# Kernel tuning notes

Hardware: AMD Instinct MI355X
Metric: run time of the kernel (lower is better)

The kernel has to match this reference:

```python
import jax, jax.numpy as jnp
import numpy as np

B, S, D, H = 2, 2048, 1024, 16
HD = D // H  # head_dim = 64
LN_EPS = 1e-5


def setup_inputs() -> dict:
    key = jax.random.key(0)
    ks = jax.random.split(key, 14)
    w = 0.02  # weight init scale
    return {
        "q": jax.random.normal(ks[0], (B, S, D), jnp.float32),
        "k": jax.random.normal(ks[1], (B, S, D), jnp.float32),
        "v": jax.random.normal(ks[2], (B, S, D), jnp.float32),
        "mask": jnp.zeros((B, 1, S, S), dtype=bool),
        "training": 0,
        "wq_w": jax.random.normal(ks[3], (D, D), jnp.float32) * w,
        "wq_b": jnp.zeros((D,), jnp.float32),
        "wk_w": jax.random.normal(ks[4], (D, D), jnp.float32) * w,
        "wk_b": jnp.zeros((D,), jnp.float32),
        "wv_w": jax.random.normal(ks[5], (D, D), jnp.float32) * w,
        "wv_b": jnp.zeros((D,), jnp.float32),
        "wo_w": jax.random.normal(ks[6], (D, D), jnp.float32) * w,
        "wo_b": jnp.zeros((D,), jnp.float32),
        "ln_g": jnp.ones((D,), jnp.float32),
        "ln_b": jnp.zeros((D,), jnp.float32),
    }


def _linear(x, w, b):
    # torch nn.Linear: x @ W.T + b, W is [out, in]
    return jnp.einsum('bsd,od->bso', x, w) + b


def _split_heads(x):
    b, s, _ = x.shape
    return x.reshape(b, s, H, HD).transpose(0, 2, 1, 3)  # [B,H,S,HD]


def reference(q, k, v, mask, training, wq_w, wq_b, wk_w, wk_b, wv_w, wv_b,
              wo_w, wo_b, ln_g, ln_b):
    residual = q
    Q = _split_heads(_linear(q, wq_w, wq_b))
    K = _split_heads(_linear(k, wk_w, wk_b))
    V = _split_heads(_linear(v, wv_w, wv_b))
    # source computes sqrt(dk) in float16, then adds 1e-8
    dk = jnp.sqrt(jnp.asarray(HD, jnp.float16)).astype(jnp.float32) + 1e-8
    score = jnp.einsum('bhqd,bhkd->bhqk', Q, K) / dk  # [B,H,S,S]
    # NOTE: source applies NO softmax; masked score is used directly.
    attn = jnp.where(mask, -jnp.inf, score)
    ctx = jnp.einsum('bhqk,bhkd->bhqd', attn, V)  # [B,H,S,HD]
    b, _, s, _ = ctx.shape
    ctx = ctx.transpose(0, 2, 1, 3).reshape(b, s, D)  # [B,S,D]
    o = _linear(ctx, wo_w, wo_b)
    # dropout is identity in eval mode
    x = residual + o
    mu = jnp.mean(x, axis=-1, keepdims=True)
    var = jnp.mean(jnp.square(x - mu), axis=-1, keepdims=True)
    return ln_g * (x - mu) * jax.lax.rsqrt(var + LN_EPS) + ln_b
```

## Files before the change

kernel.cpp:

```cpp
#include <hip/hip_runtime.h>


typedef __bf16 bf16;
typedef __bf16 bf16x8 __attribute__((ext_vector_type(8)));
typedef float f32x4 __attribute__((ext_vector_type(4)));

#define MFMA16(a, b, c) __builtin_amdgcn_mfma_f32_16x16x32_bf16(a, b, c, 0, 0, 0)

__device__ __forceinline__ bf16x8 ld8(const bf16* p) { return *(const bf16x8*)p; }

__device__ __forceinline__ void gload16(const void* g, void* l) {
  __builtin_amdgcn_global_load_lds((__attribute__((address_space(1))) void*)(g),
                                   (__attribute__((address_space(3))) void*)(l), 16, 0, 0);
}

__global__ __launch_bounds__(256) void cvt_kernel(
    const float* __restrict__ q, const float* __restrict__ k, const float* __restrict__ v,
    const float* __restrict__ wq, const float* __restrict__ wk, const float* __restrict__ wv,
    bf16* __restrict__ dst) {
  const int bid = blockIdx.x;
  const float* s; size_t dof; int x;
  if (bid < 6144) {
    const int y = bid >> 11; x = bid & 2047;
    s = (y == 0) ? q : (y == 1 ? k : v);
    dof = (size_t)y * 4194304u;
  } else {
    const int idx = bid - 6144; const int y = idx >> 9; x = idx & 511;
    s = (y == 0) ? wq : (y == 1 ? wk : wv);
    dof = 12582912u + (size_t)y * 1048576u;
  }
  const size_t i = ((size_t)x * 256 + threadIdx.x) * 8;
  f32x4 a = *(const f32x4*)(s + i);
  f32x4 b = *(const f32x4*)(s + i + 4);
  bf16x8 o;
  o[0] = (bf16)a[0]; o[1] = (bf16)a[1]; o[2] = (bf16)a[2]; o[3] = (bf16)a[3];
  o[4] = (bf16)b[0]; o[5] = (bf16)b[1]; o[6] = (bf16)b[2]; o[7] = (bf16)b[3];
  *(bf16x8*)(dst + dof + i) = o;
}

__global__ __launch_bounds__(128, 2) void gemm_proj_f(
    const bf16* __restrict__ Aall, const bf16* __restrict__ Wall,
    const float* __restrict__ bq, const float* __restrict__ bk, const float* __restrict__ bv,
    bf16* __restrict__ Call) {
  __shared__ __align__(128) char lds[32768];
  const int z = blockIdx.y;
  const int wg = blockIdx.x;
  const int swz = ((wg & 7) << 5) + (wg >> 3);
  const int n0 = (swz & 7) * 128, m0 = (swz >> 3) * 128;
  const bf16* A = Aall + (size_t)z * 4194304u;
  const bf16* W = Wall + (size_t)z * 1048576u;
  const float* bias = (z == 0) ? bq : (z == 1 ? bk : bv);
  bf16* C = Call + (size_t)z * 4194304u;

  const int t = threadIdx.x;
  const int l = t & 63, wid = t >> 6;
  const int r16 = l & 15, kg = l >> 4;
  const int wbase = wid << 10;

  const bf16* ap[4]; const bf16* bp[4]; int adst[4], bdst[4];
#pragma unroll
  for (int p = 0; p < 4; p++) {
    const int row = p * 32 + (t >> 2);
    const int c = (t & 3) ^ (row & 3) ^ ((row >> 2) & 3);
    ap[p] = A + (size_t)(m0 + row) * 1024 + c * 8;
    bp[p] = W + (size_t)(n0 + row) * 1024 + c * 8;
    adst[p] = p * 2048 + wbase;
    bdst[p] = 8192 + p * 2048 + wbase;
  }
  int aoff[8], boff[4];
#pragma unroll
  for (int i = 0; i < 8; i++) {
    const int row = i * 16 + r16;
    aoff[i] = row * 64 + ((kg ^ (row & 3) ^ ((row >> 2) & 3)) << 4);
  }
#pragma unroll
  for (int j = 0; j < 4; j++) {
    const int row = wid * 64 + j * 16 + r16;
    boff[j] = 8192 + row * 64 + ((kg ^ (row & 3) ^ ((row >> 2) & 3)) << 4);
  }

  f32x4 acc[8][4] = {};
#pragma unroll
  for (int p = 0; p < 4; p++) { gload16(ap[p], lds + adst[p]); gload16(bp[p], lds + bdst[p]); }
  __syncthreads();

  int buf = 0;
  for (int kt = 0; kt < 32; kt++) {
    if (kt < 31) {
      char* d = lds + ((buf ^ 1) << 14);
#pragma unroll
      for (int p = 0; p < 4; p++) {
        gload16(ap[p] + (kt + 1) * 32, d + adst[p]);
        gload16(bp[p] + (kt + 1) * 32, d + bdst[p]);
      }
    }
    const char* lb = lds + (buf << 14);
    bf16x8 bv_[4];
#pragma unroll
    for (int j = 0; j < 4; j++) bv_[j] = *(const bf16x8*)(lb + boff[j]);
#pragma unroll
    for (int i = 0; i < 8; i++) {
      bf16x8 av = *(const bf16x8*)(lb + aoff[i]);
#pragma unroll
      for (int j = 0; j < 4; j++) acc[i][j] = MFMA16(av, bv_[j], acc[i][j]);
    }
    __syncthreads();
    buf ^= 1;
  }

#pragma unroll
  for (int j = 0; j < 4; j++) {
    const int col = n0 + wid * 64 + j * 16 + r16;
    const float bj = bias[col];
#pragma unroll
    for (int i = 0; i < 8; i++) {
      const int row = m0 + i * 16 + kg * 4;
#pragma unroll
      for (int r = 0; r < 4; r++)
        C[(size_t)(row + r) * 1024 + col] = (bf16)(acc[i][j][r] + bj);
    }
  }
}

__device__ __forceinline__ void gemm_loop(const bf16* __restrict__ A,
                                          const bf16* __restrict__ Bw,
                                          int m0, int n0, char* lds, f32x4 acc[4][4]) {
  const int t = threadIdx.x;
  const int l = t & 63, w = t >> 6;
  const int wr = w >> 1, wc = w & 1;
  const int r16 = l & 15, kg = l >> 4;
  const int sw = ((kg ^ (r16 & 3) ^ ((r16 >> 2) & 3)) << 4);
  const int aoff = wr * 4096 + r16 * 64 + sw;
  const int boff = 8192 + wc * 4096 + r16 * 64 + sw;

  const int srow = t >> 2;
  const int k16 = (t & 3) ^ (srow & 3) ^ ((srow >> 2) & 3);
  const bf16* gA = A + (size_t)(m0 + srow) * 1024 + k16 * 8;
  const bf16* gB = Bw + (size_t)(n0 + srow) * 1024 + k16 * 8;
  const int wbase = (t >> 6) << 10;

  gload16(gA, lds + wbase);
  gload16(gA + 65536, lds + 4096 + wbase);
  gload16(gB, lds + 8192 + wbase);
  gload16(gB + 65536, lds + 12288 + wbase);
  __syncthreads();

  int buf = 0;
  for (int kt = 0; kt < 32; kt++) {
    if (kt < 31) {
      const bf16* ga = gA + (kt + 1) * 32;
      const bf16* gb = gB + (kt + 1) * 32;
      char* dst = lds + ((buf ^ 1) << 14) + wbase;
      gload16(ga, dst);
      gload16(ga + 65536, dst + 4096);
      gload16(gb, dst + 8192);
      gload16(gb + 65536, dst + 12288);
    }
    const char* la = lds + (buf << 14) + aoff;
    const char* lb = lds + (buf << 14) + boff;
    bf16x8 av[4], bv[4];
#pragma unroll
    for (int i = 0; i < 4; i++) av[i] = *(const bf16x8*)(la + i * 1024);
#pragma unroll
    for (int j = 0; j < 4; j++) bv[j] = *(const bf16x8*)(lb + j * 1024);
#pragma unroll
    for (int i = 0; i < 4; i++)
#pragma unroll
      for (int j = 0; j < 4; j++) acc[i][j] = MFMA16(av[i], bv[j], acc[i][j]);
    __syncthreads();
    buf ^= 1;
  }
}

__global__ __launch_bounds__(256) void ktv_kernel(
    const bf16* __restrict__ Kb, const bf16* __restrict__ Vb, float* __restrict__ M) {
  const int bh = blockIdx.y, b = bh >> 4, h = bh & 15;
  const int s0 = blockIdx.x * 128;
  __shared__ bf16 Kl[64][136];
  __shared__ bf16 Vl[64][136];
  const int t = threadIdx.x;
  const size_t base = ((size_t)b * 2048 + s0) * 1024 + h * 64;
#pragma unroll
  for (int p = 0; p < 4; p++) {
    const int chunk = p * 256 + t;
    const int s = chunk >> 3, d0 = (chunk & 7) * 8;
    bf16x8 kv = ld8(Kb + base + (size_t)s * 1024 + d0);
    bf16x8 vv = ld8(Vb + base + (size_t)s * 1024 + d0);
#pragma unroll
    for (int e = 0; e < 8; e++) { Kl[d0 + e][s] = kv[e]; Vl[d0 + e][s] = vv[e]; }
  }
  __syncthreads();
  const int l = t & 63, w = t >> 6;
  const int r16 = l & 15, kg = l >> 4;
  f32x4 acc[4] = {};
#pragma unroll
  for (int ks = 0; ks < 4; ks++) {
    bf16x8 a = ld8(&Kl[w * 16 + r16][ks * 32 + kg * 8]);
#pragma unroll
    for (int j = 0; j < 4; j++) {
      bf16x8 bvv = ld8(&Vl[j * 16 + r16][ks * 32 + kg * 8]);
      acc[j] = MFMA16(a, bvv, acc[j]);
    }
  }
  float* Mh = M + (size_t)bh * 4096;
#pragma unroll
  for (int j = 0; j < 4; j++)
#pragma unroll
    for (int r = 0; r < 4; r++)
      atomicAdd(&Mh[(w * 16 + kg * 4 + r) * 64 + j * 16 + r16], acc[j][r]);
}

__global__ __launch_bounds__(256) void gt_kernel(
    const float* __restrict__ Wo, const float* __restrict__ M, bf16* __restrict__ Gt) {
  const int bid = blockIdx.x;
  const int b = bid >> 7, h = (bid >> 3) & 15, nt = bid & 7;
  const int n0 = nt * 128;
  const float* Mh = M + (size_t)((b << 4) + h) * 4096;
  const int l = threadIdx.x & 63, w = threadIdx.x >> 6;
  const int r16 = l & 15, kg = l >> 4;
  f32x4 acc[2][4] = {};
#pragma unroll
  for (int kk = 0; kk < 2; kk++) {
    bf16x8 a[2];
#pragma unroll
    for (int i = 0; i < 2; i++) {
      const float* wp = Wo + (size_t)(n0 + w * 32 + i * 16 + r16) * 1024 + h * 64 + kk * 32 + kg * 8;
      f32x4 lo = *(const f32x4*)wp;
      f32x4 hi = *(const f32x4*)(wp + 4);
      a[i][0] = (bf16)lo[0]; a[i][1] = (bf16)lo[1]; a[i][2] = (bf16)lo[2]; a[i][3] = (bf16)lo[3];
      a[i][4] = (bf16)hi[0]; a[i][5] = (bf16)hi[1]; a[i][6] = (bf16)hi[2]; a[i][7] = (bf16)hi[3];
    }
#pragma unroll
    for (int j = 0; j < 4; j++) {
      const float* mp = Mh + (j * 16 + r16) * 64 + kk * 32 + kg * 8;
      f32x4 m0v = *(const f32x4*)mp;
      f32x4 m1v = *(const f32x4*)(mp + 4);
      bf16x8 bv;
      bv[0] = (bf16)(m0v[0] * 0.125f); bv[1] = (bf16)(m0v[1] * 0.125f);
      bv[2] = (bf16)(m0v[2] * 0.125f); bv[3] = (bf16)(m0v[3] * 0.125f);
      bv[4] = (bf16)(m1v[0] * 0.125f); bv[5] = (bf16)(m1v[1] * 0.125f);
      bv[6] = (bf16)(m1v[2] * 0.125f); bv[7] = (bf16)(m1v[3] * 0.125f);
#pragma unroll
      for (int i = 0; i < 2; i++) acc[i][j] = MFMA16(a[i], bv, acc[i][j]);
    }
  }
  bf16* G = Gt + (size_t)b * 1048576u;
#pragma unroll
  for (int i = 0; i < 2; i++)
#pragma unroll
    for (int j = 0; j < 4; j++)
#pragma unroll
      for (int r = 0; r < 4; r++)
        G[(size_t)(n0 + w * 32 + i * 16 + kg * 4 + r) * 1024 + h * 64 + j * 16 + r16] =
            (bf16)acc[i][j][r];
}

__global__ __launch_bounds__(256) void gemm_out(
    const bf16* __restrict__ Q, const bf16* __restrict__ Gt,
    const float* __restrict__ bo, const float* __restrict__ resid, float* __restrict__ out) {
  __shared__ __align__(128) char lds[32768];
  const int wg = blockIdx.x;
  const int swz = ((wg & 7) << 5) + (wg >> 3);
  const int n0 = (swz & 7) * 128, m0 = (swz >> 3) * 128;
  const bf16* B = Gt + (size_t)(m0 >> 11) * 1048576u;

  f32x4 acc[4][4] = {};
  gemm_loop(Q, B, m0, n0, lds, acc);

  const int l = threadIdx.x & 63, w = threadIdx.x >> 6;
  const int wr = w >> 1, wc = w & 1, r16 = l & 15, kg = l >> 4;
#pragma unroll
  for (int j = 0; j < 4; j++) {
    const int col = n0 + wc * 64 + j * 16 + r16;
    const float bj = bo[col];
#pragma unroll
    for (int i = 0; i < 4; i++) {
      const int row = m0 + wr * 64 + i * 16 + kg * 4;
#pragma unroll
      for (int r = 0; r < 4; r++) {
        const size_t off = (size_t)(row + r) * 1024 + col;
        out[off] = acc[i][j][r] + bj + resid[off];
      }
    }
  }
}

__global__ __launch_bounds__(256) void ln_kernel(
    float* __restrict__ x, const float* __restrict__ g, const float* __restrict__ bb) {
  const int lane = threadIdx.x & 63, wid = threadIdx.x >> 6;
  const int row = (blockIdx.x << 2) + wid;
  float* xr = x + (size_t)row * 1024;
  f32x4 v[4];
  float s = 0.f, s2 = 0.f;
#pragma unroll
  for (int e = 0; e < 4; e++) {
    v[e] = *(const f32x4*)(xr + lane * 16 + e * 4);
#pragma unroll
    for (int u = 0; u < 4; u++) { s += v[e][u]; s2 += v[e][u] * v[e][u]; }
  }
#pragma unroll
  for (int m = 32; m; m >>= 1) { s += __shfl_xor(s, m); s2 += __shfl_xor(s2, m); }
  const float mu = s * (1.0f / 1024.0f);
  const float rstd = rsqrtf(s2 * (1.0f / 1024.0f) - mu * mu + 1e-5f);
#pragma unroll
  for (int e = 0; e < 4; e++) {
    f32x4 gg = *(const f32x4*)(g + lane * 16 + e * 4);
    f32x4 bv = *(const f32x4*)(bb + lane * 16 + e * 4);
    f32x4 o;
#pragma unroll
    for (int u = 0; u < 4; u++) o[u] = gg[u] * ((v[e][u] - mu) * rstd) + bv[u];
    *(f32x4*)(xr + lane * 16 + e * 4) = o;
  }
}

extern "C" void kernel_launch(void* const* d_in, const int* in_sizes, int n_in,
                              void* d_out, int out_size, void* d_ws, size_t ws_size,
                              hipStream_t stream) {
  (void)in_sizes; (void)n_in; (void)out_size; (void)ws_size;
  const float* q    = (const float*)d_in[0];
  const float* k    = (const float*)d_in[1];
  const float* v    = (const float*)d_in[2];
  const float* wq_w = (const float*)d_in[5];
  const float* wq_b = (const float*)d_in[6];
  const float* wk_w = (const float*)d_in[7];
  const float* wk_b = (const float*)d_in[8];
  const float* wv_w = (const float*)d_in[9];
  const float* wv_b = (const float*)d_in[10];
  const float* wo_w = (const float*)d_in[11];
  const float* wo_b = (const float*)d_in[12];
  const float* ln_g = (const float*)d_in[13];
  const float* ln_b = (const float*)d_in[14];
  float* out = (float*)d_out;

  bf16* wsb    = (bf16*)d_ws;
  bf16* qkv_bf = wsb;
  bf16* w_bf   = wsb + 12582912u;
  bf16* QKV_bf = wsb + 15728640u;
  float* M     = (float*)wsb;
  bf16* Gt     = wsb + 524288u;

  cvt_kernel<<<7680, 256, 0, stream>>>(q, k, v, wq_w, wk_w, wv_w, wsb);
  gemm_proj_f<<<dim3(256, 3), 128, 0, stream>>>(qkv_bf, w_bf, wq_b, wk_b, wv_b, QKV_bf);
  hipMemsetAsync(M, 0, 32 * 64 * 64 * sizeof(float), stream);
  ktv_kernel<<<dim3(16, 32), 256, 0, stream>>>(QKV_bf + 4194304u, QKV_bf + 8388608u, M);
  gt_kernel<<<256, 256, 0, stream>>>(wo_w, M, Gt);
  gemm_out<<<256, 256, 0, stream>>>(QKV_bf, Gt, wo_b, q, out);
  ln_kernel<<<1024, 256, 0, stream>>>(out, ln_g, ln_b);
}
```

Baseline: 104.8 us.

## Use triple-buffered LDS ring pipeline for projection and output GEMMs, fold memset into cvt

Replaces the double-buffered GEMM main loops with a shared three-stage LDS ring that uses explicit vmcnt waits and raw barriers, so two tiles stay in flight while one is computed, and raises MFMA priority around the inner product. The QKV projection is reorganised into 768 blocks of 256 threads with 128x128 tiles and an occupancy hint of 3, in place of 128-thread blocks in a 3D grid. The memset of the M accumulator is folded into extra blocks of the conversion kernel, which removes one launch. The cost is more LDS per block (48KB) and a finer-grained synchronisation scheme that relies on vmcnt counting being correct.

```diff
diff --git a/kernel.cpp b/kernel.cpp
--- a/kernel.cpp
+++ b/kernel.cpp
@@ -6,6 +6,8 @@
 typedef float f32x4 __attribute__((ext_vector_type(4)));
 
 #define MFMA16(a, b, c) __builtin_amdgcn_mfma_f32_16x16x32_bf16(a, b, c, 0, 0, 0)
+#define VMCNT(n) asm volatile("s_waitcnt vmcnt(" #n ")" ::: "memory")
+#define BARRIER() asm volatile("s_barrier" ::: "memory")
 
 __device__ __forceinline__ bf16x8 ld8(const bf16* p) { return *(const bf16x8*)p; }
 
@@ -14,11 +16,21 @@
                                    (__attribute__((address_space(3))) void*)(l), 16, 0, 0);
 }
 
+__device__ __forceinline__ int swz_slot(int row, int c) {
+  return c ^ (row & 3) ^ ((row >> 2) & 3);
+}
+
 __global__ __launch_bounds__(256) void cvt_kernel(
     const float* __restrict__ q, const float* __restrict__ k, const float* __restrict__ v,
     const float* __restrict__ wq, const float* __restrict__ wk, const float* __restrict__ wv,
-    bf16* __restrict__ dst) {
+    bf16* __restrict__ dst, float* __restrict__ Mz) {
   const int bid = blockIdx.x;
+  if (bid >= 7680) {
+    float* p = Mz + (size_t)(bid - 7680) * 2048 + threadIdx.x * 8;
+    *(f32x4*)p = f32x4{0.f, 0.f, 0.f, 0.f};
+    *(f32x4*)(p + 4) = f32x4{0.f, 0.f, 0.f, 0.f};
+    return;
+  }
   const float* s; size_t dof; int x;
   if (bid < 6144) {
     const int y = bid >> 11; x = bid & 2047;
@@ -38,137 +50,103 @@
   *(bf16x8*)(dst + dof + i) = o;
 }
 
-__global__ __launch_bounds__(128, 2) void gemm_proj_f(
-    const bf16* __restrict__ Aall, const bf16* __restrict__ Wall,
+__device__ __forceinline__ void compute16(const char* buf, const int aoff[4], const int boff[4],
+                                          f32x4 (&acc)[4][4]) {
+  bf16x8 av[4], bv[4];
+#pragma unroll
+  for (int i = 0; i < 4; i++) av[i] = *(const bf16x8*)(buf + aoff[i]);
+#pragma unroll
+  for (int j = 0; j < 4; j++) bv[j] = *(const bf16x8*)(buf + boff[j]);
+  __builtin_amdgcn_s_setprio(1);
+#pragma unroll
+  for (int i = 0; i < 4; i++)
+#pragma unroll
+    for (int j = 0; j < 4; j++) acc[i][j] = MFMA16(av[i], bv[j], acc[i][j]);
+  __builtin_amdgcn_s_setprio(0);
+}
+
+__device__ __forceinline__ void ring128(const bf16* __restrict__ A, const bf16* __restrict__ B,
+                                        char* lds, f32x4 (&acc)[4][4]) {
+  const int t = threadIdx.x;
+  const int lane = t & 63, wid = t >> 6;
+  const int wr = wid >> 1, wc = wid & 1;
+  const int r16 = lane & 15, kg = lane >> 4;
+
+  int aoff[4], boff[4];
+#pragma unroll
+  for (int i = 0; i < 4; i++) {
+    int row = wr * 64 + i * 16 + r16;
+    aoff[i] = row * 64 + (swz_slot(row, kg) << 4);
+    row = wc * 64 + i * 16 + r16;
+    boff[i] = 8192 + row * 64 + (swz_slot(row, kg) << 4);
+  }
+
+  const int r1 = t >> 2, c = t & 3, r2 = r1 + 64;
+  const bf16* pa1 = A + (size_t)r1 * 1024 + swz_slot(r1, c) * 8;
+  const bf16* pa2 = A + (size_t)r2 * 1024 + swz_slot(r2, c) * 8;
+  const bf16* pb1 = B + (size_t)r1 * 1024 + swz_slot(r1, c) * 8;
+  const bf16* pb2 = B + (size_t)r2 * 1024 + swz_slot(r2, c) * 8;
+  const int d1 = wid << 10, d2 = 4096 + (wid << 10);
+
+#pragma unroll
+  for (int p = 0; p < 2; p++) {
+    char* d = lds + p * 16384;
+    gload16(pa1 + p * 32, d + d1);
+    gload16(pa2 + p * 32, d + d2);
+    gload16(pb1 + p * 32, d + 8192 + d1);
+    gload16(pb2 + p * 32, d + 8192 + d2);
+  }
+  pa1 += 64; pa2 += 64; pb1 += 64; pb2 += 64;
+
+  int cb = 0, rb = 2;
+  for (int kt = 0; kt < 30; kt++) {
+    VMCNT(4);
+    BARRIER();
+    {
+      char* d = lds + rb * 16384;
+      gload16(pa1, d + d1);
+      gload16(pa2, d + d2);
+      gload16(pb1, d + 8192 + d1);
+      gload16(pb2, d + 8192 + d2);
+      pa1 += 32; pa2 += 32; pb1 += 32; pb2 += 32;
+    }
+    compute16(lds + cb * 16384, aoff, boff, acc);
+    cb = (cb == 2) ? 0 : cb + 1;
+    rb = (rb == 2) ? 0 : rb + 1;
+  }
+  VMCNT(4); BARRIER(); compute16(lds + cb * 16384, aoff, boff, acc);
+  cb = (cb == 2) ? 0 : cb + 1;
+  VMCNT(0); BARRIER(); compute16(lds + cb * 16384, aoff, boff, acc);
+}
+
+__global__ __launch_bounds__(256, 3) void gemm_proj_r(
+    const bf16* __restrict__ qkv, const bf16* __restrict__ Wall,
     const float* __restrict__ bq, const float* __restrict__ bk, const float* __restrict__ bv,
     bf16* __restrict__ Call) {
-  __shared__ __align__(128) char lds[32768];
-  const int z = blockIdx.y;
+  __shared__ __align__(1024) char lds[49152];
   const int wg = blockIdx.x;
-  const int swz = ((wg & 7) << 5) + (wg >> 3);
-  const int n0 = (swz & 7) * 128, m0 = (swz >> 3) * 128;
-  const bf16* A = Aall + (size_t)z * 4194304u;
-  const bf16* W = Wall + (size_t)z * 1048576u;
+  const int swz = (wg & 7) * 96 + (wg >> 3);
+  const int mt = swz >> 3, nt = swz & 7;
+  const int m0 = mt * 128, n0 = nt * 128;
+  const int z = m0 >> 12;
+
+  f32x4 acc[4][4] = {};
+  ring128(qkv + (size_t)m0 * 1024, Wall + (size_t)z * 1048576u + (size_t)n0 * 1024, lds, acc);
+
   const float* bias = (z == 0) ? bq : (z == 1 ? bk : bv);
-  bf16* C = Call + (size_t)z * 4194304u;
-
-  const int t = threadIdx.x;
-  const int l = t & 63, wid = t >> 6;
-  const int r16 = l & 15, kg = l >> 4;
-  const int wbase = wid << 10;
-
-  const bf16* ap[4]; const bf16* bp[4]; int adst[4], bdst[4];
-#pragma unroll
-  for (int p = 0; p < 4; p++) {
-    const int row = p * 32 + (t >> 2);
-    const int c = (t & 3) ^ (row & 3) ^ ((row >> 2) & 3);
-    ap[p] = A + (size_t)(m0 + row) * 1024 + c * 8;
-    bp[p] = W + (size_t)(n0 + row) * 1024 + c * 8;
-    adst[p] = p * 2048 + wbase;
-    bdst[p] = 8192 + p * 2048 + wbase;
-  }
-  int aoff[8], boff[4];
-#pragma unroll
-  for (int i = 0; i < 8; i++) {
-    const int row = i * 16 + r16;
-    aoff[i] = row * 64 + ((kg ^ (row & 3) ^ ((row >> 2) & 3)) << 4);
-  }
+  const int lane = threadIdx.x & 63, wid = threadIdx.x >> 6;
+  const int wr = wid >> 1, wc = wid & 1, r16 = lane & 15, kg = lane >> 4;
 #pragma unroll
   for (int j = 0; j < 4; j++) {
-    const int row = wid * 64 + j * 16 + r16;
-    boff[j] = 8192 + row * 64 + ((kg ^ (row & 3) ^ ((row >> 2) & 3)) << 4);
-  }
-
-  f32x4 acc[8][4] = {};
-#pragma unroll
-  for (int p = 0; p < 4; p++) { gload16(ap[p], lds + adst[p]); gload16(bp[p], lds + bdst[p]); }
-  __syncthreads();
-
-  int buf = 0;
-  for (int kt = 0; kt < 32; kt++) {
-    if (kt < 31) {
-      char* d = lds + ((buf ^ 1) << 14);
-#pragma unroll
-      for (int p = 0; p < 4; p++) {
-        gload16(ap[p] + (kt + 1) * 32, d + adst[p]);
-        gload16(bp[p] + (kt + 1) * 32, d + bdst[p]);
-      }
-    }
-    const char* lb = lds + (buf << 14);
-    bf16x8 bv_[4];
-#pragma unroll
-    for (int j = 0; j < 4; j++) bv_[j] = *(const bf16x8*)(lb + boff[j]);
-#pragma unroll
-    for (int i = 0; i < 8; i++) {
-      bf16x8 av = *(const bf16x8*)(lb + aoff[i]);
-#pragma unroll
-      for (int j = 0; j < 4; j++) acc[i][j] = MFMA16(av, bv_[j], acc[i][j]);
-    }
-    __syncthreads();
-    buf ^= 1;
-  }
-
-#pragma unroll
-  for (int j = 0; j < 4; j++) {
-    const int col = n0 + wid * 64 + j * 16 + r16;
+    const int col = n0 + wc * 64 + j * 16 + r16;
     const float bj = bias[col];
 #pragma unroll
-    for (int i = 0; i < 8; i++) {
-      const int row = m0 + i * 16 + kg * 4;
+    for (int i = 0; i < 4; i++) {
+      const int row = m0 + wr * 64 + i * 16 + kg * 4;
 #pragma unroll
       for (int r = 0; r < 4; r++)
-        C[(size_t)(row + r) * 1024 + col] = (bf16)(acc[i][j][r] + bj);
-    }
-  }
-}
-
-__device__ __forceinline__ void gemm_loop(const bf16* __restrict__ A,
-                                          const bf16* __restrict__ Bw,
-                                          int m0, int n0, char* lds, f32x4 acc[4][4]) {
-  const int t = threadIdx.x;
-  const int l = t & 63, w = t >> 6;
-  const int wr = w >> 1, wc = w & 1;
-  const int r16 = l & 15, kg = l >> 4;
-  const int sw = ((kg ^ (r16 & 3) ^ ((r16 >> 2) & 3)) << 4);
-  const int aoff = wr * 4096 + r16 * 64 + sw;
-  const int boff = 8192 + wc * 4096 + r16 * 64 + sw;
-
-  const int srow = t >> 2;
-  const int k16 = (t & 3) ^ (srow & 3) ^ ((srow >> 2) & 3);
-  const bf16* gA = A + (size_t)(m0 + srow) * 1024 + k16 * 8;
-  const bf16* gB = Bw + (size_t)(n0 + srow) * 1024 + k16 * 8;
-  const int wbase = (t >> 6) << 10;
-
-  gload16(gA, lds + wbase);
-  gload16(gA + 65536, lds + 4096 + wbase);
-  gload16(gB, lds + 8192 + wbase);
-  gload16(gB + 65536, lds + 12288 + wbase);
-  __syncthreads();
-
-  int buf = 0;
-  for (int kt = 0; kt < 32; kt++) {
-    if (kt < 31) {
-      const bf16* ga = gA + (kt + 1) * 32;
-      const bf16* gb = gB + (kt + 1) * 32;
-      char* dst = lds + ((buf ^ 1) << 14) + wbase;
-      gload16(ga, dst);
-      gload16(ga + 65536, dst + 4096);
-      gload16(gb, dst + 8192);
-      gload16(gb + 65536, dst + 12288);
-    }
-    const char* la = lds + (buf << 14) + aoff;
-    const char* lb = lds + (buf << 14) + boff;
-    bf16x8 av[4], bv[4];
-#pragma unroll
-    for (int i = 0; i < 4; i++) av[i] = *(const bf16x8*)(la + i * 1024);
-#pragma unroll
-    for (int j = 0; j < 4; j++) bv[j] = *(const bf16x8*)(lb + j * 1024);
-#pragma unroll
-    for (int i = 0; i < 4; i++)
-#pragma unroll
-      for (int j = 0; j < 4; j++) acc[i][j] = MFMA16(av[i], bv[j], acc[i][j]);
-    __syncthreads();
-    buf ^= 1;
+        Call[(size_t)(row + r) * 1024 + col] = (bf16)(acc[i][j][r] + bj);
+    }
   }
 }
 
@@ -255,20 +233,20 @@
             (bf16)acc[i][j][r];
 }
 
-__global__ __launch_bounds__(256) void gemm_out(
+__global__ __launch_bounds__(256, 3) void gemm_out_r(
     const bf16* __restrict__ Q, const bf16* __restrict__ Gt,
     const float* __restrict__ bo, const float* __restrict__ resid, float* __restrict__ out) {
-  __shared__ __align__(128) char lds[32768];
+  __shared__ __align__(1024) char lds[49152];
   const int wg = blockIdx.x;
-  const int swz = ((wg & 7) << 5) + (wg >> 3);
-  const int n0 = (swz & 7) * 128, m0 = (swz >> 3) * 128;
-  const bf16* B = Gt + (size_t)(m0 >> 11) * 1048576u;
+  const int swz = (wg & 7) * 32 + (wg >> 3);
+  const int mt = swz >> 3, nt = swz & 7;
+  const int m0 = mt * 128, n0 = nt * 128;
 
   f32x4 acc[4][4] = {};
-  gemm_loop(Q, B, m0, n0, lds, acc);
-
-  const int l = threadIdx.x & 63, w = threadIdx.x >> 6;
-  const int wr = w >> 1, wc = w & 1, r16 = l & 15, kg = l >> 4;
+  ring128(Q + (size_t)m0 * 1024, Gt + (size_t)(m0 >> 11) * 1048576u + (size_t)n0 * 1024, lds, acc);
+
+  const int lane = threadIdx.x & 63, wid = threadIdx.x >> 6;
+  const int wr = wid >> 1, wc = wid & 1, r16 = lane & 15, kg = lane >> 4;
 #pragma unroll
   for (int j = 0; j < 4; j++) {
     const int col = n0 + wc * 64 + j * 16 + r16;
@@ -336,14 +314,13 @@
   bf16* qkv_bf = wsb;
   bf16* w_bf   = wsb + 12582912u;
   bf16* QKV_bf = wsb + 15728640u;
-  float* M     = (float*)wsb;
-  bf16* Gt     = wsb + 524288u;
-
-  cvt_kernel<<<7680, 256, 0, stream>>>(q, k, v, wq_w, wk_w, wv_w, wsb);
-  gemm_proj_f<<<dim3(256, 3), 128, 0, stream>>>(qkv_bf, w_bf, wq_b, wk_b, wv_b, QKV_bf);
-  hipMemsetAsync(M, 0, 32 * 64 * 64 * sizeof(float), stream);
+  float* M     = (float*)(wsb + 28311552u);
+  bf16* Gt     = wsb;
+
+  cvt_kernel<<<7744, 256, 0, stream>>>(q, k, v, wq_w, wk_w, wv_w, qkv_bf, M);
+  gemm_proj_r<<<768, 256, 0, stream>>>(qkv_bf, w_bf, wq_b, wk_b, wv_b, QKV_bf);
   ktv_kernel<<<dim3(16, 32), 256, 0, stream>>>(QKV_bf + 4194304u, QKV_bf + 8388608u, M);
   gt_kernel<<<256, 256, 0, stream>>>(wo_w, M, Gt);
-  gemm_out<<<256, 256, 0, stream>>>(QKV_bf, Gt, wo_b, q, out);
+  gemm_out_r<<<256, 256, 0, stream>>>(QKV_bf, Gt, wo_b, q, out);
   ln_kernel<<<1024, 256, 0, stream>>>(out, ln_g, ln_b);
 }
```

After: 96.24 us. 1.09x faster.
